# Kernel tuning notes

Measured on AMD Instinct MI355X. Metric: run time of the kernel, lower is better.

## Reference

```python
import jax, jax.numpy as jnp
import numpy as np

G = 4
EPS = 1e-5

def group_norm(x, gamma, beta):
    B, C, D, H, W = x.shape
    xg = x.reshape(B, G, C // G, D, H, W)
    mu = xg.mean(axis=(2, 3, 4, 5), keepdims=True)
    var = xg.var(axis=(2, 3, 4, 5), keepdims=True)
    xn = ((xg - mu) * jax.lax.rsqrt(var + EPS)).reshape(B, C, D, H, W)
    return xn * gamma[None, :, None, None, None] + beta[None, :, None, None, None]

def conv3d(x, w, b):
    y = jax.lax.conv_general_dilated(x, w, (1, 1, 1), [(1, 1), (1, 1), (1, 1)],
                                     dimension_numbers=('NCDHW', 'OIDHW', 'NCDHW'))
    return y + b[None, :, None, None, None]

def deform_conv_hw(x, offset, w, b):
    # x: [B,C,D,H,W]; offset: [B, 2*27, D,H,W] -> per-tap (dh, dw); depth taps are rigid.
    B, C, D, H, W = x.shape
    off = offset.reshape(B, 27, 2, D, H, W)
    xp = jnp.pad(x, ((0, 0), (0, 0), (1, 1), (0, 0), (0, 0)))  # zero-pad depth only
    hh = jnp.arange(H, dtype=x.dtype)[None, None, :, None]
    ww = jnp.arange(W, dtype=x.dtype)[None, None, None, :]
    bi = jnp.arange(B)[:, None, None, None]
    di = jnp.arange(D)[None, :, None, None]
    out = jnp.zeros((B, w.shape[0], D, H, W), x.dtype)
    tap = 0
    for i in range(3):
        x_d = xp[:, :, i:i + D]  # depth-shifted view [B,C,D,H,W]
        for j in range(3):
            for k in range(3):
                hp = hh + (j - 1) + off[:, tap, 0]  # [B,D,H,W] fractional h position
                wp = ww + (k - 1) + off[:, tap, 1]
                h0 = jnp.floor(hp); w0 = jnp.floor(wp)
                h0i = h0.astype(jnp.int32); w0i = w0.astype(jnp.int32)
                lh = hp - h0; lw = wp - w0
                def gather(hi, wi):
                    m = ((hi >= 0) & (hi < H) & (wi >= 0) & (wi < W)).astype(x.dtype)
                    g = x_d[bi, :, di, jnp.clip(hi, 0, H - 1), jnp.clip(wi, 0, W - 1)]  # [B,D,H,W,C]
                    return g, m
                g00, m00 = gather(h0i, w0i)
                g01, m01 = gather(h0i, w0i + 1)
                g10, m10 = gather(h0i + 1, w0i)
                g11, m11 = gather(h0i + 1, w0i + 1)
                val = (((1 - lh) * (1 - lw) * m00)[..., None] * g00
                       + ((1 - lh) * lw * m01)[..., None] * g01
                       + (lh * (1 - lw) * m10)[..., None] * g10
                       + (lh * lw * m11)[..., None] * g11)
                out = out + jnp.einsum('bdhwc,oc->bodhw', val, w[:, :, i, j, k])
                tap += 1
    return out + b[None, :, None, None, None]

def setup_inputs():
    key = jax.random.key(0)
    ks = jax.random.split(key, 8)
    B, C, D, H, W = 1, 32, 24, 96, 96
    x = jax.random.normal(ks[0], (B, C, D, H, W), jnp.float32)
    g1 = jnp.ones((C,), jnp.float32); be1 = jnp.zeros((C,), jnp.float32)
    g2 = jnp.ones((C,), jnp.float32); be2 = jnp.zeros((C,), jnp.float32)
    ow1 = jax.random.normal(ks[1], (54, C, 3, 3, 3), jnp.float32) * 0.02
    ob1 = jnp.zeros((54,), jnp.float32)
    dw1 = jax.random.normal(ks[2], (C, C, 3, 3, 3), jnp.float32) * 0.05
    db1 = jnp.zeros((C,), jnp.float32)
    ow2 = jax.random.normal(ks[3], (54, C, 3, 3, 3), jnp.float32) * 0.02
    ob2 = jnp.zeros((54,), jnp.float32)
    dw2 = jax.random.normal(ks[4], (C, C, 3, 3, 3), jnp.float32) * 0.05
    db2 = jnp.zeros((C,), jnp.float32)
    return {"x": x, "g1": g1, "be1": be1, "g2": g2, "be2": be2,
            "ow1": ow1, "ob1": ob1, "dw1": dw1, "db1": db1,
            "ow2": ow2, "ob2": ob2, "dw2": dw2, "db2": db2}

def reference(x, g1, be1, g2, be2, ow1, ob1, dw1, db1, ow2, ob2, dw2, db2):
    h = jax.nn.relu(group_norm(x, g1, be1))
    h = deform_conv_hw(h, conv3d(h, ow1, ob1), dw1, db1)
    h = jax.nn.relu(group_norm(h, g2, be2))
    h = deform_conv_hw(h, conv3d(h, ow2, ob2), dw2, db2)
    return h + x
```

## Files before the change

### kernel.cpp

```cpp
#include <hip/hip_runtime.h>
#include <hip/hip_fp16.h>

#define CC   32
#define DD   24
#define HH   96
#define WW   96
#define HWC  (HH*WW)
#define DHW  (DD*HH*WW)
#define NG   4
#define CPG  (CC/NG)
#define OC1  54
#define GN_EPS 1e-5f
#define NBLK2 (DHW/128)
#define CHUNK2 (NBLK2/8)

typedef float  f32x4 __attribute__((ext_vector_type(4)));
typedef _Float16 f16x8 __attribute__((ext_vector_type(8)));
typedef unsigned int u32x4 __attribute__((ext_vector_type(4)));

union F16Frag { f16x8 v; __half2 h2[4]; };

__device__ __forceinline__ int swz_block(int bid) {
    return (bid % 8) * CHUNK2 + (bid / 8);
}

__global__ void pack_w(const float* __restrict__ src, _Float16* __restrict__ dst,
                       int O, int NT, int n) {
    int idx = blockIdx.x * 256 + threadIdx.x;
    if (idx >= n) return;
    int e    = idx & 7;
    int lane = (idx >> 3) & 63;
    int nt   = (idx >> 9) % NT;
    int tap  = (idx >> 9) / NT;
    int o = nt * 16 + (lane & 15);
    int c = (lane >> 4) * 8 + e;
    float v = (o < O) ? src[(o * CC + c) * 27 + tap] : 0.f;
    dst[idx] = (_Float16)v;
}

__global__ void gn_stats(const float* __restrict__ x, float* __restrict__ stats) {
    const int g = blockIdx.x >> 5;
    const int s = blockIdx.x & 31;
    const float4* base = (const float4*)(x + (size_t)g * CPG * DHW);
    const int n4 = CPG * DHW / 4;
    float s1 = 0.f, s2 = 0.f;
    for (int idx = s * 256 + threadIdx.x; idx < n4; idx += 32 * 256) {
        float4 v = base[idx];
        s1 += v.x + v.y + v.z + v.w;
        s2 += v.x * v.x + v.y * v.y + v.z * v.z + v.w * v.w;
    }
    for (int off = 32; off > 0; off >>= 1) {
        s1 += __shfl_down(s1, off);
        s2 += __shfl_down(s2, off);
    }
    __shared__ float ls1[4], ls2[4];
    int wid = threadIdx.x >> 6;
    if ((threadIdx.x & 63) == 0) { ls1[wid] = s1; ls2[wid] = s2; }
    __syncthreads();
    if (threadIdx.x == 0) {
        float a = 0.f, b = 0.f;
        for (int i = 0; i < 4; i++) { a += ls1[i]; b += ls2[i]; }
        atomicAdd(&stats[g * 2 + 0], a);
        atomicAdd(&stats[g * 2 + 1], b);
    }
}

__global__ void gn_apply_T(const float* __restrict__ x, const float* __restrict__ stats,
                           const float* __restrict__ gamma, const float* __restrict__ beta,
                           __half* __restrict__ yT) {
    const int p = blockIdx.x * 256 + threadIdx.x;
    const float invN = 1.0f / (float)(CPG * DHW);
    float mean[NG], rstd[NG];
#pragma unroll
    for (int g = 0; g < NG; g++) {
        mean[g] = stats[2 * g] * invN;
        float var = stats[2 * g + 1] * invN - mean[g] * mean[g];
        rstd[g] = rsqrtf(var + GN_EPS);
    }
    float vals[CC];
#pragma unroll
    for (int c = 0; c < CC; c++) {
        const int g = c >> 3;
        const float ga = gamma[c] * rstd[g];
        const float be = beta[c] - mean[g] * ga;
        vals[c] = fmaxf(0.f, x[(size_t)c * DHW + p] * ga + be);
    }
    union { __half2 h2[16]; u32x4 q[4]; } u;
#pragma unroll
    for (int c = 0; c < 16; c++) u.h2[c] = __floats2half2_rn(vals[2 * c], vals[2 * c + 1]);
    u32x4* dst = (u32x4*)(yT + (size_t)p * CC);
#pragma unroll
    for (int q = 0; q < 4; q++) __builtin_nontemporal_store(u.q[q], dst + q);
}

__global__ __launch_bounds__(128) void offs_mfma(const __half* __restrict__ xT,
                                                 const _Float16* __restrict__ wB,
                                                 const float* __restrict__ bias,
                                                 __half* __restrict__ offF) {
    const int tid  = threadIdx.x;
    const int lane = tid & 63;
    const int wave = tid >> 6;
    const int p0   = swz_block(blockIdx.x) * 128;
    const int pw   = p0 + wave * 64;
    const int d    = pw / HWC;
    const int rem  = pw % HWC;
    const int mrow = lane & 15;
    const int kg   = lane >> 4;

    int hq[4], wq[4];
#pragma unroll
    for (int m = 0; m < 4; m++) {
        int rr = rem + m * 16 + mrow;
        hq[m] = rr / WW; wq[m] = rr % WW;
    }

    f32x4 acc[4][4];
#pragma unroll
    for (int m = 0; m < 4; m++)
#pragma unroll
        for (int n = 0; n < 4; n++) acc[m][n] = (f32x4){0.f, 0.f, 0.f, 0.f};

    const f16x8* wb8 = (const f16x8*)wB;

#pragma unroll 1
    for (int i = 0; i < 3; i++) {
        const int dd = d + i - 1;
        if ((unsigned)dd >= DD) continue;
        const __half* xd = xT + (size_t)dd * HWC * CC;
#pragma unroll 1
        for (int jk = 0; jk < 9; jk++) {
            const int j = jk / 3, k = jk % 3, tap = i * 9 + jk;
            const f16x8 b0 = wb8[(tap * 4 + 0) * 64 + lane];
            const f16x8 b1 = wb8[(tap * 4 + 1) * 64 + lane];
            const f16x8 b2 = wb8[(tap * 4 + 2) * 64 + lane];
            const f16x8 b3 = wb8[(tap * 4 + 3) * 64 + lane];
#pragma unroll
            for (int m = 0; m < 4; m++) {
                const int hh = hq[m] + j - 1;
                const int ww = wq[m] + k - 1;
                f16x8 a = {0, 0, 0, 0, 0, 0, 0, 0};
                if ((unsigned)hh < HH && (unsigned)ww < WW)
                    a = *(const f16x8*)(xd + (size_t)(hh * WW + ww) * CC + kg * 8);
                acc[m][0] = __builtin_amdgcn_mfma_f32_16x16x32_f16(a, b0, acc[m][0], 0, 0, 0);
                acc[m][1] = __builtin_amdgcn_mfma_f32_16x16x32_f16(a, b1, acc[m][1], 0, 0, 0);
                acc[m][2] = __builtin_amdgcn_mfma_f32_16x16x32_f16(a, b2, acc[m][2], 0, 0, 0);
                acc[m][3] = __builtin_amdgcn_mfma_f32_16x16x32_f16(a, b3, acc[m][3], 0, 0, 0);
            }
        }
    }

    __shared__ __align__(16) float lds[OC1 * 132];
#pragma unroll
    for (int m = 0; m < 4; m++)
#pragma unroll
        for (int nt = 0; nt < 4; nt++) {
            int o = nt * 16 + mrow;
            if (o < OC1)
                *(f32x4*)&lds[o * 132 + wave * 64 + m * 16 + kg * 4] = acc[m][nt];
        }
    __syncthreads();
#pragma unroll 1
    for (int o = 0; o < OC1; o++) {
        float v = lds[o * 132 + tid] + bias[o];
        offF[(size_t)o * DHW + p0 + tid] = __float2half(v);
    }
}

__global__ __launch_bounds__(128) void deform_mfma(const __half* __restrict__ xT,
                                                   const __half* __restrict__ offF,
                                                   const _Float16* __restrict__ wB,
                                                   const float* __restrict__ bias,
                                                   const float* __restrict__ resid,
                                                   float* __restrict__ outp) {
    const int tid  = threadIdx.x;
    const int lane = tid & 63;
    const int wave = tid >> 6;
    const int p0   = swz_block(blockIdx.x) * 128;
    const int pw   = p0 + wave * 64;
    const int d    = pw / HWC;
    const int rem  = pw % HWC;
    const int mrow = lane & 15;
    const int kg   = lane >> 4;

    int hq[4], wq[4];
#pragma unroll
    for (int m = 0; m < 4; m++) {
        int rr = rem + m * 16 + mrow;
        hq[m] = rr / WW; wq[m] = rr % WW;
    }

    f32x4 acc[4][2];
#pragma unroll
    for (int m = 0; m < 4; m++) {
        acc[m][0] = (f32x4){0.f, 0.f, 0.f, 0.f};
        acc[m][1] = (f32x4){0.f, 0.f, 0.f, 0.f};
    }

    const f16x8* wb8 = (const f16x8*)wB;

#pragma unroll 1
    for (int i = 0; i < 3; i++) {
        const int dd = d + i - 1;
        if ((unsigned)dd >= DD) continue;
        const __half* xd = xT + (size_t)dd * HWC * CC;
#pragma unroll 1
        for (int jk = 0; jk < 9; jk++) {
            const int j = jk / 3, k = jk % 3, tap = i * 9 + jk;
            const f16x8 b0 = wb8[(tap * 2 + 0) * 64 + lane];
            const f16x8 b1 = wb8[(tap * 2 + 1) * 64 + lane];
            const __half* offh = offF + (size_t)(tap * 2 + 0) * DHW;
            const __half* offw = offF + (size_t)(tap * 2 + 1) * DHW;
#pragma unroll
            for (int m = 0; m < 4; m++) {
                const int pq = pw + m * 16 + mrow;
                const float oh = __half2float(offh[pq]);
                const float ov = __half2float(offw[pq]);
                const float hp  = (float)(hq[m] + j - 1) + oh;
                const float wpf = (float)(wq[m] + k - 1) + ov;
                const float h0f = floorf(hp), w0f = floorf(wpf);
                const int h0 = (int)h0f, w0 = (int)w0f;
                const float lh = hp - h0f, lw = wpf - w0f;
                const bool hv0 = (h0 >= 0) && (h0 < HH);
                const bool hv1 = (h0 >= -1) && (h0 < HH - 1);
                const bool wv0 = (w0 >= 0) && (w0 < WW);
                const bool wv1 = (w0 >= -1) && (w0 < WW - 1);
                const float c00 = (hv0 && wv0) ? (1.f - lh) * (1.f - lw) : 0.f;
                const float c01 = (hv0 && wv1) ? (1.f - lh) * lw : 0.f;
                const float c10 = (hv1 && wv0) ? lh * (1.f - lw) : 0.f;
                const float c11 = (hv1 && wv1) ? lh * lw : 0.f;
                const int h0c = min(max(h0, 0), HH - 1);
                const int h1c = min(max(h0 + 1, 0), HH - 1);
                const int w0c = min(max(w0, 0), WW - 1);
                const int w1c = min(max(w0 + 1, 0), WW - 1);
                F16Frag a00, a01, a10, a11, A;
                a00.v = *(const f16x8*)(xd + (size_t)(h0c * WW + w0c) * CC + kg * 8);
                a01.v = *(const f16x8*)(xd + (size_t)(h0c * WW + w1c) * CC + kg * 8);
                a10.v = *(const f16x8*)(xd + (size_t)(h1c * WW + w0c) * CC + kg * 8);
                a11.v = *(const f16x8*)(xd + (size_t)(h1c * WW + w1c) * CC + kg * 8);
                const __half2 C00 = __float2half2_rn(c00);
                const __half2 C01 = __float2half2_rn(c01);
                const __half2 C10 = __float2half2_rn(c10);
                const __half2 C11 = __float2half2_rn(c11);
#pragma unroll
                for (int r = 0; r < 4; r++) {
                    __half2 t = __hmul2(C00, a00.h2[r]);
                    t = __hfma2(C01, a01.h2[r], t);
                    t = __hfma2(C10, a10.h2[r], t);
                    t = __hfma2(C11, a11.h2[r], t);
                    A.h2[r] = t;
                }
                acc[m][0] = __builtin_amdgcn_mfma_f32_16x16x32_f16(A.v, b0, acc[m][0], 0, 0, 0);
                acc[m][1] = __builtin_amdgcn_mfma_f32_16x16x32_f16(A.v, b1, acc[m][1], 0, 0, 0);
            }
        }
    }

    __shared__ __align__(16) float lds[CC * 132];
#pragma unroll
    for (int m = 0; m < 4; m++)
#pragma unroll
        for (int nt = 0; nt < 2; nt++) {
            int o = nt * 16 + mrow;
            *(f32x4*)&lds[o * 132 + wave * 64 + m * 16 + kg * 4] = acc[m][nt];
        }
    __syncthreads();
    if (resid) {
#pragma unroll 1
        for (int o = 0; o < CC; o++) {
            float v = lds[o * 132 + tid] + bias[o] + resid[(size_t)o * DHW + p0 + tid];
            outp[(size_t)o * DHW + p0 + tid] = v;
        }
    } else {
#pragma unroll 1
        for (int o = 0; o < CC; o++) {
            float v = lds[o * 132 + tid] + bias[o];
            outp[(size_t)o * DHW + p0 + tid] = v;
        }
    }
}

extern "C" void kernel_launch(void* const* d_in, const int* in_sizes, int n_in,
                              void* d_out, int out_size, void* d_ws, size_t ws_size,
                              hipStream_t stream) {
    const float* x   = (const float*)d_in[0];
    const float* g1  = (const float*)d_in[1];
    const float* be1 = (const float*)d_in[2];
    const float* g2  = (const float*)d_in[3];
    const float* be2 = (const float*)d_in[4];
    const float* ow1 = (const float*)d_in[5];
    const float* ob1 = (const float*)d_in[6];
    const float* dw1 = (const float*)d_in[7];
    const float* db1 = (const float*)d_in[8];
    const float* ow2 = (const float*)d_in[9];
    const float* ob2 = (const float*)d_in[10];
    const float* dw2 = (const float*)d_in[11];
    const float* db2 = (const float*)d_in[12];
    float* out = (float*)d_out;
    float* ws  = (float*)d_ws;

    float*    stats = ws;
    _Float16* wBo1  = (_Float16*)(ws + 256);
    _Float16* wBd1  = (_Float16*)(ws + 27904);
    _Float16* wBo2  = (_Float16*)(ws + 41728);
    _Float16* wBd2  = (_Float16*)(ws + 69376);
    __half*   hT    = (__half*)(ws + 83200);
    __half*   offF  = (__half*)(ws + 3622144);

    (void)hipMemsetAsync(stats, 0, 16 * sizeof(float), stream);
    pack_w<<<(27 * 4 * 512 + 255) / 256, 256, 0, stream>>>(ow1, wBo1, 54, 4, 27 * 4 * 512);
    pack_w<<<(27 * 2 * 512 + 255) / 256, 256, 0, stream>>>(dw1, wBd1, 32, 2, 27 * 2 * 512);
    pack_w<<<(27 * 4 * 512 + 255) / 256, 256, 0, stream>>>(ow2, wBo2, 54, 4, 27 * 4 * 512);
    pack_w<<<(27 * 2 * 512 + 255) / 256, 256, 0, stream>>>(dw2, wBd2, 32, 2, 27 * 2 * 512);

    gn_stats<<<NG * 32, 256, 0, stream>>>(x, stats + 0);
    gn_apply_T<<<DHW / 256, 256, 0, stream>>>(x, stats + 0, g1, be1, hT);
    offs_mfma<<<NBLK2, 128, 0, stream>>>(hT, wBo1, ob1, offF);
    deform_mfma<<<NBLK2, 128, 0, stream>>>(hT, offF, wBd1, db1, nullptr, out);

    gn_stats<<<NG * 32, 256, 0, stream>>>(out, stats + 8);
    gn_apply_T<<<DHW / 256, 256, 0, stream>>>(out, stats + 8, g2, be2, hT);
    offs_mfma<<<NBLK2, 128, 0, stream>>>(hT, wBo2, ob2, offF);
    deform_mfma<<<NBLK2, 128, 0, stream>>>(hT, offF, wBd2, db2, x, out);
}
```

Baseline: 426.7 us.

## Split deform taps across waves, store offsets pixel-major, swizzle GN blocks

Several changes land together. The deform kernel now gives each 128-thread block 64 pixels, splits the 27 taps between its two waves, and sums the partial accumulators through LDS. This doubles the block count and raises the occupancy hint. The offset conv now writes its 54 channels pixel-major as packed half2 (converted through a half-precision LDS stage) so that deform reads each (dh, dw) pair with one 32-bit load. gn_apply gets a block swizzle and drops nontemporal stores so its output stays in cache, and the offs tap loop is partially unrolled. The cost is an extra LDS reduction and sync in deform, plus a second fp16 rounding of the offsets before the bias is added.

```diff
diff --git a/kernel.cpp b/kernel.cpp
--- a/kernel.cpp
+++ b/kernel.cpp
@@ -11,8 +11,13 @@
 #define CPG  (CC/NG)
 #define OC1  54
 #define GN_EPS 1e-5f
-#define NBLK2 (DHW/128)
-#define CHUNK2 (NBLK2/8)
+
+#define NBLK_O (DHW/128)
+#define CHUNK_O (NBLK_O/8)
+#define NBLK_D (DHW/64)
+#define CHUNK_D (NBLK_D/8)
+#define NBLK_G (DHW/256)
+#define CHUNK_G (NBLK_G/8)
 
 typedef float  f32x4 __attribute__((ext_vector_type(4)));
 typedef _Float16 f16x8 __attribute__((ext_vector_type(8)));
@@ -20,8 +25,8 @@
 
 union F16Frag { f16x8 v; __half2 h2[4]; };
 
-__device__ __forceinline__ int swz_block(int bid) {
-    return (bid % 8) * CHUNK2 + (bid / 8);
+__device__ __forceinline__ int swz(int bid, int chunk) {
+    return (bid % 8) * chunk + (bid / 8);
 }
 
 __global__ void pack_w(const float* __restrict__ src, _Float16* __restrict__ dst,
@@ -68,7 +73,7 @@
 __global__ void gn_apply_T(const float* __restrict__ x, const float* __restrict__ stats,
                            const float* __restrict__ gamma, const float* __restrict__ beta,
                            __half* __restrict__ yT) {
-    const int p = blockIdx.x * 256 + threadIdx.x;
+    const int p = swz(blockIdx.x, CHUNK_G) * 256 + threadIdx.x;
     const float invN = 1.0f / (float)(CPG * DHW);
     float mean[NG], rstd[NG];
 #pragma unroll
@@ -90,17 +95,17 @@
     for (int c = 0; c < 16; c++) u.h2[c] = __floats2half2_rn(vals[2 * c], vals[2 * c + 1]);
     u32x4* dst = (u32x4*)(yT + (size_t)p * CC);
 #pragma unroll
-    for (int q = 0; q < 4; q++) __builtin_nontemporal_store(u.q[q], dst + q);
+    for (int q = 0; q < 4; q++) dst[q] = u.q[q];
 }
 
 __global__ __launch_bounds__(128) void offs_mfma(const __half* __restrict__ xT,
                                                  const _Float16* __restrict__ wB,
                                                  const float* __restrict__ bias,
-                                                 __half* __restrict__ offF) {
+                                                 __half* __restrict__ offC) {
     const int tid  = threadIdx.x;
     const int lane = tid & 63;
     const int wave = tid >> 6;
-    const int p0   = swz_block(blockIdx.x) * 128;
+    const int p0   = swz(blockIdx.x, CHUNK_O) * 128;
     const int pw   = p0 + wave * 64;
     const int d    = pw / HWC;
     const int rem  = pw % HWC;
@@ -127,7 +132,7 @@
         const int dd = d + i - 1;
         if ((unsigned)dd >= DD) continue;
         const __half* xd = xT + (size_t)dd * HWC * CC;
-#pragma unroll 1
+#pragma unroll 3
         for (int jk = 0; jk < 9; jk++) {
             const int j = jk / 3, k = jk % 3, tap = i * 9 + jk;
             const f16x8 b0 = wb8[(tap * 4 + 0) * 64 + lane];
@@ -149,36 +154,44 @@
         }
     }
 
-    __shared__ __align__(16) float lds[OC1 * 132];
-#pragma unroll
-    for (int m = 0; m < 4; m++)
+    __shared__ __half lds_h[OC1 * 136];
+#pragma unroll
+    for (int m = 0; m < 4; m++) {
 #pragma unroll
         for (int nt = 0; nt < 4; nt++) {
-            int o = nt * 16 + mrow;
-            if (o < OC1)
-                *(f32x4*)&lds[o * 132 + wave * 64 + m * 16 + kg * 4] = acc[m][nt];
-        }
+            const int o = nt * 16 + mrow;
+            if (o < OC1) {
+                const int idx = o * 136 + wave * 64 + m * 16 + kg * 4;
+                __half2 lo = __floats2half2_rn(acc[m][nt].x, acc[m][nt].y);
+                __half2 hi = __floats2half2_rn(acc[m][nt].z, acc[m][nt].w);
+                *(__half2*)&lds_h[idx]     = lo;
+                *(__half2*)&lds_h[idx + 2] = hi;
+            }
+        }
+    }
     __syncthreads();
+    unsigned int* dst = (unsigned int*)(offC + (size_t)(p0 + tid) * 54);
 #pragma unroll 1
-    for (int o = 0; o < OC1; o++) {
-        float v = lds[o * 132 + tid] + bias[o];
-        offF[(size_t)o * DHW + p0 + tid] = __float2half(v);
-    }
-}
-
-__global__ __launch_bounds__(128) void deform_mfma(const __half* __restrict__ xT,
-                                                   const __half* __restrict__ offF,
-                                                   const _Float16* __restrict__ wB,
-                                                   const float* __restrict__ bias,
-                                                   const float* __restrict__ resid,
-                                                   float* __restrict__ outp) {
+    for (int o2 = 0; o2 < 27; o2++) {
+        float f0 = __half2float(lds_h[(2 * o2 + 0) * 136 + tid]) + bias[2 * o2 + 0];
+        float f1 = __half2float(lds_h[(2 * o2 + 1) * 136 + tid]) + bias[2 * o2 + 1];
+        __half2 r = __floats2half2_rn(f0, f1);
+        dst[o2] = *(unsigned int*)&r;
+    }
+}
+
+__global__ __launch_bounds__(128, 6) void deform_mfma(const __half* __restrict__ xT,
+                                                      const __half* __restrict__ offC,
+                                                      const _Float16* __restrict__ wB,
+                                                      const float* __restrict__ bias,
+                                                      const float* __restrict__ resid,
+                                                      float* __restrict__ outp) {
     const int tid  = threadIdx.x;
     const int lane = tid & 63;
     const int wave = tid >> 6;
-    const int p0   = swz_block(blockIdx.x) * 128;
-    const int pw   = p0 + wave * 64;
-    const int d    = pw / HWC;
-    const int rem  = pw % HWC;
+    const int p0   = swz(blockIdx.x, CHUNK_D) * 64;
+    const int d    = p0 / HWC;
+    const int rem  = p0 % HWC;
     const int mrow = lane & 15;
     const int kg   = lane >> 4;
 
@@ -199,82 +212,101 @@
     const f16x8* wb8 = (const f16x8*)wB;
 
 #pragma unroll 1
-    for (int i = 0; i < 3; i++) {
+    for (int t3 = wave; t3 < 27; t3 += 2) {
+        const int i = t3 / 9;
         const int dd = d + i - 1;
         if ((unsigned)dd >= DD) continue;
+        const int jk = t3 % 9;
+        const int j = jk / 3, k = jk % 3;
         const __half* xd = xT + (size_t)dd * HWC * CC;
-#pragma unroll 1
-        for (int jk = 0; jk < 9; jk++) {
-            const int j = jk / 3, k = jk % 3, tap = i * 9 + jk;
-            const f16x8 b0 = wb8[(tap * 2 + 0) * 64 + lane];
-            const f16x8 b1 = wb8[(tap * 2 + 1) * 64 + lane];
-            const __half* offh = offF + (size_t)(tap * 2 + 0) * DHW;
-            const __half* offw = offF + (size_t)(tap * 2 + 1) * DHW;
-#pragma unroll
-            for (int m = 0; m < 4; m++) {
-                const int pq = pw + m * 16 + mrow;
-                const float oh = __half2float(offh[pq]);
-                const float ov = __half2float(offw[pq]);
-                const float hp  = (float)(hq[m] + j - 1) + oh;
-                const float wpf = (float)(wq[m] + k - 1) + ov;
-                const float h0f = floorf(hp), w0f = floorf(wpf);
-                const int h0 = (int)h0f, w0 = (int)w0f;
-                const float lh = hp - h0f, lw = wpf - w0f;
-                const bool hv0 = (h0 >= 0) && (h0 < HH);
-                const bool hv1 = (h0 >= -1) && (h0 < HH - 1);
-                const bool wv0 = (w0 >= 0) && (w0 < WW);
-                const bool wv1 = (w0 >= -1) && (w0 < WW - 1);
-                const float c00 = (hv0 && wv0) ? (1.f - lh) * (1.f - lw) : 0.f;
-                const float c01 = (hv0 && wv1) ? (1.f - lh) * lw : 0.f;
-                const float c10 = (hv1 && wv0) ? lh * (1.f - lw) : 0.f;
-                const float c11 = (hv1 && wv1) ? lh * lw : 0.f;
-                const int h0c = min(max(h0, 0), HH - 1);
-                const int h1c = min(max(h0 + 1, 0), HH - 1);
-                const int w0c = min(max(w0, 0), WW - 1);
-                const int w1c = min(max(w0 + 1, 0), WW - 1);
-                F16Frag a00, a01, a10, a11, A;
-                a00.v = *(const f16x8*)(xd + (size_t)(h0c * WW + w0c) * CC + kg * 8);
-                a01.v = *(const f16x8*)(xd + (size_t)(h0c * WW + w1c) * CC + kg * 8);
-                a10.v = *(const f16x8*)(xd + (size_t)(h1c * WW + w0c) * CC + kg * 8);
-                a11.v = *(const f16x8*)(xd + (size_t)(h1c * WW + w1c) * CC + kg * 8);
-                const __half2 C00 = __float2half2_rn(c00);
-                const __half2 C01 = __float2half2_rn(c01);
-                const __half2 C10 = __float2half2_rn(c10);
-                const __half2 C11 = __float2half2_rn(c11);
-#pragma unroll
-                for (int r = 0; r < 4; r++) {
-                    __half2 t = __hmul2(C00, a00.h2[r]);
-                    t = __hfma2(C01, a01.h2[r], t);
-                    t = __hfma2(C10, a10.h2[r], t);
-                    t = __hfma2(C11, a11.h2[r], t);
-                    A.h2[r] = t;
-                }
-                acc[m][0] = __builtin_amdgcn_mfma_f32_16x16x32_f16(A.v, b0, acc[m][0], 0, 0, 0);
-                acc[m][1] = __builtin_amdgcn_mfma_f32_16x16x32_f16(A.v, b1, acc[m][1], 0, 0, 0);
-            }
-        }
-    }
-
-    __shared__ __align__(16) float lds[CC * 132];
-#pragma unroll
-    for (int m = 0; m < 4; m++)
-#pragma unroll
-        for (int nt = 0; nt < 2; nt++) {
-            int o = nt * 16 + mrow;
-            *(f32x4*)&lds[o * 132 + wave * 64 + m * 16 + kg * 4] = acc[m][nt];
-        }
+        const f16x8 b0 = wb8[(t3 * 2 + 0) * 64 + lane];
+        const f16x8 b1 = wb8[(t3 * 2 + 1) * 64 + lane];
+#pragma unroll
+        for (int m = 0; m < 4; m++) {
+            const int pq = p0 + m * 16 + mrow;
+            const unsigned int ou =
+                *(const unsigned int*)((const char*)offC + ((size_t)pq * 54 + 2 * t3) * 2);
+            const __half2 o2 = *(const __half2*)&ou;
+            const float oh = __half2float(__low2half(o2));
+            const float ov = __half2float(__high2half(o2));
+            const float hp  = (float)(hq[m] + j - 1) + oh;
+            const float wpf = (float)(wq[m] + k - 1) + ov;
+            const float h0f = floorf(hp), w0f = floorf(wpf);
+            const int h0 = (int)h0f, w0 = (int)w0f;
+            const float lh = hp - h0f, lw = wpf - w0f;
+            const bool hv0 = (h0 >= 0) && (h0 < HH);
+            const bool hv1 = (h0 >= -1) && (h0 < HH - 1);
+            const bool wv0 = (w0 >= 0) && (w0 < WW);
+            const bool wv1 = (w0 >= -1) && (w0 < WW - 1);
+            const float c00 = (hv0 && wv0) ? (1.f - lh) * (1.f - lw) : 0.f;
+            const float c01 = (hv0 && wv1) ? (1.f - lh) * lw : 0.f;
+            const float c10 = (hv1 && wv0) ? lh * (1.f - lw) : 0.f;
+            const float c11 = (hv1 && wv1) ? lh * lw : 0.f;
+            const int h0c = min(max(h0, 0), HH - 1);
+            const int h1c = min(max(h0 + 1, 0), HH - 1);
+            const int w0c = min(max(w0, 0), WW - 1);
+            const int w1c = min(max(w0 + 1, 0), WW - 1);
+            F16Frag a00, a01, a10, a11, A;
+            a00.v = *(const f16x8*)(xd + (size_t)(h0c * WW + w0c) * CC + kg * 8);
+            a01.v = *(const f16x8*)(xd + (size_t)(h0c * WW + w1c) * CC + kg * 8);
+            a10.v = *(const f16x8*)(xd + (size_t)(h1c * WW + w0c) * CC + kg * 8);
+            a11.v = *(const f16x8*)(xd + (size_t)(h1c * WW + w1c) * CC + kg * 8);
+            const __half2 C00 = __float2half2_rn(c00);
+            const __half2 C01 = __float2half2_rn(c01);
+            const __half2 C10 = __float2half2_rn(c10);
+            const __half2 C11 = __float2half2_rn(c11);
+#pragma unroll
+            for (int r = 0; r < 4; r++) {
+                __half2 t = __hmul2(C00, a00.h2[r]);
+                t = __hfma2(C01, a01.h2[r], t);
+                t = __hfma2(C10, a10.h2[r], t);
+                t = __hfma2(C11, a11.h2[r], t);
+                A.h2[r] = t;
+            }
+            acc[m][0] = __builtin_amdgcn_mfma_f32_16x16x32_f16(A.v, b0, acc[m][0], 0, 0, 0);
+            acc[m][1] = __builtin_amdgcn_mfma_f32_16x16x32_f16(A.v, b1, acc[m][1], 0, 0, 0);
+        }
+    }
+
+    __shared__ __align__(16) float red[CC * 68];
+    if (wave == 1) {
+#pragma unroll
+        for (int m = 0; m < 4; m++)
+#pragma unroll
+            for (int nt = 0; nt < 2; nt++) {
+                const int o = nt * 16 + mrow;
+                *(f32x4*)&red[o * 68 + m * 16 + kg * 4] = acc[m][nt];
+            }
+    }
     __syncthreads();
+    if (wave == 0) {
+#pragma unroll
+        for (int m = 0; m < 4; m++)
+#pragma unroll
+            for (int nt = 0; nt < 2; nt++) {
+                const int o = nt * 16 + mrow;
+                const int idx = o * 68 + m * 16 + kg * 4;
+                f32x4 v = *(f32x4*)&red[idx];
+                v.x += acc[m][nt].x; v.y += acc[m][nt].y;
+                v.z += acc[m][nt].z; v.w += acc[m][nt].w;
+                *(f32x4*)&red[idx] = v;
+            }
+    }
+    __syncthreads();
+    const int pp  = tid & 63;
+    const int ob  = tid >> 6;
     if (resid) {
-#pragma unroll 1
-        for (int o = 0; o < CC; o++) {
-            float v = lds[o * 132 + tid] + bias[o] + resid[(size_t)o * DHW + p0 + tid];
-            outp[(size_t)o * DHW + p0 + tid] = v;
+#pragma unroll
+        for (int o2 = 0; o2 < 16; o2++) {
+            const int o = o2 * 2 + ob;
+            float v = red[o * 68 + pp] + bias[o] + resid[(size_t)o * DHW + p0 + pp];
+            outp[(size_t)o * DHW + p0 + pp] = v;
         }
     } else {
-#pragma unroll 1
-        for (int o = 0; o < CC; o++) {
-            float v = lds[o * 132 + tid] + bias[o];
-            outp[(size_t)o * DHW + p0 + tid] = v;
+#pragma unroll
+        for (int o2 = 0; o2 < 16; o2++) {
+            const int o = o2 * 2 + ob;
+            outp[(size_t)o * DHW + p0 + pp] = red[o * 68 + pp] + bias[o];
         }
     }
 }
@@ -304,7 +336,7 @@
     _Float16* wBo2  = (_Float16*)(ws + 41728);
     _Float16* wBd2  = (_Float16*)(ws + 69376);
     __half*   hT    = (__half*)(ws + 83200);
-    __half*   offF  = (__half*)(ws + 3622144);
+    __half*   offC  = (__half*)(ws + 3622144);
 
     (void)hipMemsetAsync(stats, 0, 16 * sizeof(float), stream);
     pack_w<<<(27 * 4 * 512 + 255) / 256, 256, 0, stream>>>(ow1, wBo1, 54, 4, 27 * 4 * 512);
@@ -313,12 +345,12 @@
     pack_w<<<(27 * 2 * 512 + 255) / 256, 256, 0, stream>>>(dw2, wBd2, 32, 2, 27 * 2 * 512);
 
     gn_stats<<<NG * 32, 256, 0, stream>>>(x, stats + 0);
-    gn_apply_T<<<DHW / 256, 256, 0, stream>>>(x, stats + 0, g1, be1, hT);
-    offs_mfma<<<NBLK2, 128, 0, stream>>>(hT, wBo1, ob1, offF);
-    deform_mfma<<<NBLK2, 128, 0, stream>>>(hT, offF, wBd1, db1, nullptr, out);
+    gn_apply_T<<<NBLK_G, 256, 0, stream>>>(x, stats + 0, g1, be1, hT);
+    offs_mfma<<<NBLK_O, 128, 0, stream>>>(hT, wBo1, ob1, offC);
+    deform_mfma<<<NBLK_D, 128, 0, stream>>>(hT, offC, wBd1, db1, nullptr, out);
 
     gn_stats<<<NG * 32, 256, 0, stream>>>(out, stats + 8);
-    gn_apply_T<<<DHW / 256, 256, 0, stream>>>(out, stats + 8, g2, be2, hT);
-    offs_mfma<<<NBLK2, 128, 0, stream>>>(hT, wBo2, ob2, offF);
-    deform_mfma<<<NBLK2, 128, 0, stream>>>(hT, offF, wBd2, db2, x, out);
-}
+    gn_apply_T<<<NBLK_G, 256, 0, stream>>>(out, stats + 8, g2, be2, hT);
+    offs_mfma<<<NBLK_O, 128, 0, stream>>>(hT, wBo2, ob2, offC);
+    deform_mfma<<<NBLK_D, 128, 0, stream>>>(hT, offC, wBd2, db2, x, out);
+}
```

Result: slower. 542.4 us (+27.1%).
